# Kernel optimization log

Hardware: AMD Instinct MI355X
Metric: run time of the kernel (lower is better)

Reference implementation:

```python
import jax, jax.numpy as jnp
import numpy as np

DIM = 1024
NUM_HEADS = 16
HEAD_DIM = DIM // NUM_HEADS
B, N = 4, 2048
ROPE_BASE = 10000.0


def _rope_cos_sin(seq_len, dim):
    # inv_freq: (dim/2,), cache layout cat([freqs, freqs], -1) as in the torch module
    inv_freq = 1.0 / (ROPE_BASE ** (jnp.arange(0, dim, 2, dtype=jnp.float32) / dim))
    t = jnp.arange(seq_len, dtype=jnp.float32)
    freqs = jnp.outer(t, inv_freq)                  # (N, dim/2)
    emb = jnp.concatenate([freqs, freqs], axis=-1)  # (N, dim)
    return jnp.cos(emb), jnp.sin(emb)


def _apply_rope(x, cos, sin):
    # x: (B, H, N, Dh); rotation interleaves even/odd lanes: stack([-x_odd, x_even]).flatten
    x_rot = jnp.stack([-x[..., 1::2], x[..., ::2]], axis=-1).reshape(x.shape)
    return x * cos + x_rot * sin


def setup_inputs() -> dict:
    key = jax.random.key(0)
    k1, k2, k3, k4, k5 = jax.random.split(key, 5)
    x = jax.random.normal(k1, (B, N, DIM), dtype=jnp.float32)
    mask = jnp.ones((B, N), dtype=jnp.int32)
    # nn.Linear weights: (out_features, in_features)
    s = 1.0 / np.sqrt(DIM)
    w_qkv = jax.random.uniform(k2, (3 * DIM, DIM), jnp.float32, -s, s)
    b_qkv = jax.random.uniform(k3, (3 * DIM,), jnp.float32, -s, s)
    w_proj = jax.random.uniform(k4, (DIM, DIM), jnp.float32, -s, s)
    b_proj = jax.random.uniform(k5, (DIM,), jnp.float32, -s, s)
    return {"x": x, "mask": mask, "w_qkv": w_qkv, "b_qkv": b_qkv,
            "w_proj": w_proj, "b_proj": b_proj}


def reference(x, mask, w_qkv, b_qkv, w_proj, b_proj):
    Bz, Nz, D = x.shape
    H, Dh = NUM_HEADS, HEAD_DIM
    scale = Dh ** -0.5
    qkv = x @ w_qkv.T + b_qkv                         # (B, N, 3D)
    qkv = qkv.reshape(Bz, Nz, 3, H, Dh)
    qkv = jnp.transpose(qkv, (2, 0, 3, 1, 4))         # (3, B, H, N, Dh)
    q, k, v = qkv[0], qkv[1], qkv[2]
    cos, sin = _rope_cos_sin(Nz, Dh)
    q = _apply_rope(q, cos, sin)
    k = _apply_rope(k, cos, sin)
    attn = jnp.einsum('bhqd,bhkd->bhqk', q, k) * scale
    attn = jnp.where(mask[:, None, None, :] == 0, -jnp.inf, attn)
    attn = jax.nn.softmax(attn, axis=-1)
    out = jnp.einsum('bhqk,bhkd->bhqd', attn, v)      # (B, H, N, Dh)
    out = jnp.transpose(out, (0, 2, 1, 3)).reshape(Bz, Nz, D)
    return out @ w_proj.T + b_proj
```

## Files before the change

### kernel.cpp

```cpp
#include <hip/hip_runtime.h>
#include <hip/hip_bf16.h>

typedef __bf16 bf16;
typedef __attribute__((ext_vector_type(8))) __bf16 bf16x8;
typedef __attribute__((ext_vector_type(4))) __bf16 bf16x4;
typedef __attribute__((ext_vector_type(4))) float f32x4;

#define MFMA16(a, b, c) __builtin_amdgcn_mfma_f32_16x16x32_bf16((a), (b), (c), 0, 0, 0)

__device__ __forceinline__ void gload16(const bf16* g, bf16* lds) {
  __builtin_amdgcn_global_load_lds(
      (const __attribute__((address_space(1))) void*)g,
      (__attribute__((address_space(3))) void*)lds, 16, 0, 0);
}

__global__ void rope_table_kernel(float* __restrict__ cosT, float* __restrict__ sinT) {
  const int n = blockIdx.x;
  const int d = threadIdx.x;
  const int i = d & 31;
  const double inv = pow(10000.0, -(double)(2 * i) / 64.0);
  const float ang = (float)n * (float)inv;
  cosT[n * 64 + d] = cosf(ang);
  sinT[n * 64 + d] = sinf(ang);
}

__global__ void maskbias_kernel(const int* __restrict__ mask, float* __restrict__ mb) {
  const int i = blockIdx.x * blockDim.x + threadIdx.x;
  if (i < 8192) mb[i] = mask[i] ? -4.3280851f : -1e30f;
}

__global__ void cast_f32_bf16(const float* __restrict__ s, bf16* __restrict__ d, int n8) {
  for (int i = blockIdx.x * blockDim.x + threadIdx.x; i < n8; i += gridDim.x * blockDim.x) {
    const float4* p = (const float4*)s + (size_t)i * 2;
    const float4 a = p[0], b = p[1];
    bf16x8 o;
    o[0] = (bf16)a.x; o[1] = (bf16)a.y; o[2] = (bf16)a.z; o[3] = (bf16)a.w;
    o[4] = (bf16)b.x; o[5] = (bf16)b.y; o[6] = (bf16)b.z; o[7] = (bf16)b.w;
    *((bf16x8*)d + i) = o;
  }
}

__device__ __forceinline__ void gemm_tile_1024(const bf16* __restrict__ ga,
                                               const bf16* __restrict__ gb,
                                               bf16* As, bf16* Bs, int t,
                                               f32x4 acc[4][4]) {
  const int l = t & 63;
  const int w = t >> 6, wr = w >> 1, wc = w & 1;
  const int lr = l & 15, lk = (l >> 4) * 8;
  const int r0 = t >> 2, c0 = (t & 3) * 8;
  for (int k0 = 0; k0 < 1024; k0 += 32) {
    gload16(ga + r0 * 1024 + k0 + c0, As + t * 8);
    gload16(ga + (r0 + 64) * 1024 + k0 + c0, As + (t + 256) * 8);
    gload16(gb + r0 * 1024 + k0 + c0, Bs + t * 8);
    gload16(gb + (r0 + 64) * 1024 + k0 + c0, Bs + (t + 256) * 8);
    __syncthreads();
    bf16x8 af[4], bfr[4];
#pragma unroll
    for (int i = 0; i < 4; i++)
      af[i] = *(const bf16x8*)(As + (wr * 64 + i * 16 + lr) * 32 + lk);
#pragma unroll
    for (int j = 0; j < 4; j++)
      bfr[j] = *(const bf16x8*)(Bs + (wc * 64 + j * 16 + lr) * 32 + lk);
#pragma unroll
    for (int i = 0; i < 4; i++)
#pragma unroll
      for (int j = 0; j < 4; j++)
        acc[i][j] = MFMA16(af[i], bfr[j], acc[i][j]);
    __syncthreads();
  }
}

__global__ __launch_bounds__(256) void qkv_rope_kernel(
    const bf16* __restrict__ Xb, const bf16* __restrict__ Wb,
    const float* __restrict__ bias, const float* __restrict__ cosT,
    const float* __restrict__ sinT, bf16* __restrict__ Qo, bf16* __restrict__ Ko,
    bf16* __restrict__ Vo) {
  __shared__ bf16 As[128 * 32];
  __shared__ bf16 Bs[128 * 32];
  __shared__ bf16 Ts[4][16 * 68];
  const int t = threadIdx.x;
  const int m0 = blockIdx.x * 128, o0 = blockIdx.y * 128;
  f32x4 acc[4][4] = {};
  gemm_tile_1024(Xb + (long)m0 * 1024, Wb + (long)o0 * 1024, As, Bs, t, acc);

  const int l = t & 63, w = t >> 6, wr = w >> 1, wc = w & 1;
  const int lr = l & 15, rb = (l >> 4) * 4;
  const int seg = o0 >> 10;
  if (seg < 2) {
    bf16* dst = seg == 0 ? Qo : Ko;
#pragma unroll
    for (int j = 0; j < 4; j++) {
      const int ocol = o0 + wc * 64 + j * 16 + lr;
      const float bv = bias[ocol];
      const int oo = ocol & 1023;
      const int h = oo >> 6, d = oo & 63;
#pragma unroll
      for (int i = 0; i < 4; i++) {
#pragma unroll
        for (int r = 0; r < 4; r++) {
          const int m = m0 + wr * 64 + i * 16 + rb + r;
          const int n = m & 2047, bb = m >> 11;
          float c = acc[i][j][r] + bv;
          const float partner = __shfl_xor(c, 1);
          const float cs = cosT[n * 64 + d], sn = sinT[n * 64 + d];
          c = (d & 1) ? fmaf(c, cs, partner * sn) : fmaf(c, cs, -partner * sn);
          dst[(((long)(bb * 16 + h)) * 2048 + n) * 64 + d] = (bf16)c;
        }
      }
    }
  } else {
    bf16* Tw = &Ts[w][0];
    const int col = l >> 2, chk = l & 3;
    const int mrow = m0 + wr * 64 + chk * 16;
    const int bb2 = mrow >> 11, n2 = mrow & 2047;
#pragma unroll
    for (int j = 0; j < 4; j++) {
      const int ocol = o0 + wc * 64 + j * 16 + lr;
      const float bv = bias[ocol];
#pragma unroll
      for (int i = 0; i < 4; i++)
#pragma unroll
        for (int r = 0; r < 4; r++)
          Tw[lr * 68 + i * 16 + rb + r] = (bf16)(acc[i][j][r] + bv);
      const int oc2 = o0 + wc * 64 + j * 16 + col;
      const int h2 = (oc2 & 1023) >> 6, d2 = oc2 & 63;
      const long vbase = (((long)(bb2 * 16 + h2)) * 64 + d2) * 2048 + n2;
      const bf16x8 v0 = *(const bf16x8*)(Tw + col * 68 + chk * 16);
      const bf16x8 v1 = *(const bf16x8*)(Tw + col * 68 + chk * 16 + 8);
      *(bf16x8*)(Vo + vbase) = v0;
      *(bf16x8*)(Vo + vbase + 8) = v1;
    }
  }
}

__global__ __launch_bounds__(256) void attn_kernel(
    const bf16* __restrict__ Q, const bf16* __restrict__ K, const bf16* __restrict__ Vt,
    const float* __restrict__ mbias, bf16* __restrict__ Aout) {
  __shared__ bf16 Ks[2][64 * 64];
  __shared__ bf16 Vs[2][64 * 64];
  __shared__ bf16 Ps[4][16 * 64];
  const int t = threadIdx.x, l = t & 63, w = t >> 6;
  const int qb = blockIdx.x & 31, h = (blockIdx.x >> 5) & 15, bb = blockIdx.x >> 9;
  const long base = ((long)(bb * 16 + h)) * 2048 * 64;
  const bf16* qp = Q + base;
  const int lr = l & 15, g = l >> 4, rb = g * 4;
  const int q0 = qb * 64 + w * 16;
  bf16* Pw = &Ps[w][0];

  int kaddr[2], pwaddr[4];
#pragma unroll
  for (int ks = 0; ks < 2; ks++) kaddr[ks] = lr * 64 + (((ks * 4 + g) ^ (lr & 7)) * 8);
#pragma unroll
  for (int ct = 0; ct < 4; ct++)
    pwaddr[ct] = lr * 64 + (((ct * 2 + (g >> 1)) ^ (lr & 7)) * 8) + (g & 1) * 4;

  const int rA = (w << 3) + (l >> 3);
  const int sl8 = ((l & 7) ^ (l >> 3)) * 8;
  const int ldsoff = rA * 64 + (l & 7) * 8;
  const bf16* kptr0 = K + base + rA * 64 + sl8;
  const bf16* kptr1 = K + base + (rA + 32) * 64 + sl8;
  const bf16* vptr0 = Vt + base + (long)rA * 2048 + sl8;
  const bf16* vptr1 = Vt + base + (long)(rA + 32) * 2048 + sl8;
  const float* mptr = mbias + bb * 2048 + rb;

  auto stageKV = [&](int buf) {
    gload16(kptr0, &Ks[buf][ldsoff]);
    gload16(kptr1, &Ks[buf][2048 + ldsoff]);
    gload16(vptr0, &Vs[buf][ldsoff]);
    gload16(vptr1, &Vs[buf][2048 + ldsoff]);
    kptr0 += 4096; kptr1 += 4096; vptr0 += 64; vptr1 += 64;
  };

  bf16x8 qf[2];
#pragma unroll
  for (int ks = 0; ks < 2; ks++)
    qf[ks] = *(const bf16x8*)(qp + (q0 + lr) * 64 + ks * 32 + g * 8);

  bf16x8 ones;
#pragma unroll
  for (int i = 0; i < 8; i++) ones[i] = (bf16)1.0f;

  f32x4 oacc[4] = {};
  f32x4 sacc = {};
  const float SCL = 0.18033688f;

  auto compute = [&](const bf16* Kb_, const bf16* Vb_, const float* mp) {
    f32x4 sf[4];
#pragma unroll
    for (int ct = 0; ct < 4; ct++) {
      sf[ct] = (f32x4){0.f, 0.f, 0.f, 0.f};
#pragma unroll
      for (int ks = 0; ks < 2; ks++) {
        const bf16x8 kf = *(const bf16x8*)(Kb_ + ct * 1024 + kaddr[ks]);
        sf[ct] = MFMA16(kf, qf[ks], sf[ct]);
      }
    }
#pragma unroll
    for (int ct = 0; ct < 4; ct++) {
      const float4 mb = *(const float4*)(mp + ct * 16);
      bf16x4 pw;
      pw[0] = (bf16)exp2f(fmaf(sf[ct][0], SCL, mb.x));
      pw[1] = (bf16)exp2f(fmaf(sf[ct][1], SCL, mb.y));
      pw[2] = (bf16)exp2f(fmaf(sf[ct][2], SCL, mb.z));
      pw[3] = (bf16)exp2f(fmaf(sf[ct][3], SCL, mb.w));
      *(bf16x4*)(Pw + pwaddr[ct]) = pw;
    }
#pragma unroll
    for (int ks = 0; ks < 2; ks++) {
      const bf16x8 pf = *(const bf16x8*)(Pw + kaddr[ks]);
      sacc = MFMA16(pf, ones, sacc);
#pragma unroll
      for (int dt = 0; dt < 4; dt++) {
        const bf16x8 vf = *(const bf16x8*)(Vb_ + dt * 1024 + kaddr[ks]);
        oacc[dt] = MFMA16(pf, vf, oacc[dt]);
      }
    }
  };

  stageKV(0);
  for (int it = 0; it < 16; ++it) {
    __syncthreads();
    stageKV(1);
    compute(&Ks[0][0], &Vs[0][0], mptr);
    mptr += 64;
    __syncthreads();
    stageKV(0);
    compute(&Ks[1][0], &Vs[1][0], mptr);
    mptr += 64;
  }

  float li[4];
#pragma unroll
  for (int r = 0; r < 4; r++) li[r] = 1.0f / sacc[r];
#pragma unroll
  for (int dt = 0; dt < 4; dt++)
#pragma unroll
    for (int r = 0; r < 4; r++) {
      const int n = q0 + rb + r;
      Aout[((long)(bb * 2048 + n)) * 1024 + h * 64 + dt * 16 + lr] =
          (bf16)(oacc[dt][r] * li[r]);
    }
}

__global__ __launch_bounds__(256) void proj_kernel(const bf16* __restrict__ Ab,
                                                   const bf16* __restrict__ Wb,
                                                   const float* __restrict__ bias,
                                                   float* __restrict__ out) {
  __shared__ bf16 As[128 * 32];
  __shared__ bf16 Bs[128 * 32];
  const int t = threadIdx.x;
  const int m0 = blockIdx.x * 128, o0 = blockIdx.y * 128;
  f32x4 acc[4][4] = {};
  gemm_tile_1024(Ab + (long)m0 * 1024, Wb + (long)o0 * 1024, As, Bs, t, acc);
  const int l = t & 63, w = t >> 6, wr = w >> 1, wc = w & 1;
  const int lr = l & 15, rb = (l >> 4) * 4;
#pragma unroll
  for (int j = 0; j < 4; j++) {
    const int ocol = o0 + wc * 64 + j * 16 + lr;
    const float bv = bias[ocol];
#pragma unroll
    for (int i = 0; i < 4; i++) {
#pragma unroll
      for (int r = 0; r < 4; r++) {
        const int m = m0 + wr * 64 + i * 16 + rb + r;
        out[(long)m * 1024 + ocol] = acc[i][j][r] + bv;
      }
    }
  }
}

extern "C" void kernel_launch(void* const* d_in, const int* in_sizes, int n_in,
                              void* d_out, int out_size, void* d_ws, size_t ws_size,
                              hipStream_t stream) {
  (void)in_sizes; (void)n_in; (void)out_size; (void)ws_size;
  const float* x = (const float*)d_in[0];
  const int* mask = (const int*)d_in[1];
  const float* w_qkv = (const float*)d_in[2];
  const float* b_qkv = (const float*)d_in[3];
  const float* w_proj = (const float*)d_in[4];
  const float* b_proj = (const float*)d_in[5];
  float* out = (float*)d_out;

  char* ws = (char*)d_ws;
  size_t off = 0;
  auto alloc = [&](size_t bytes) -> void* {
    void* p = ws + off;
    off += (bytes + 255) & ~(size_t)255;
    return p;
  };
  float* cosT = (float*)alloc((size_t)2048 * 64 * 4);
  float* sinT = (float*)alloc((size_t)2048 * 64 * 4);
  float* mbias = (float*)alloc((size_t)8192 * 4);
  bf16* xb = (bf16*)alloc((size_t)8192 * 1024 * 2);
  bf16* wqkvb = (bf16*)alloc((size_t)3072 * 1024 * 2);
  bf16* wprojb = (bf16*)alloc((size_t)1024 * 1024 * 2);
  bf16* Qb = (bf16*)alloc((size_t)8388608 * 2);
  bf16* Kb = (bf16*)alloc((size_t)8388608 * 2);
  bf16* Vb = (bf16*)alloc((size_t)8388608 * 2);
  bf16* A2 = (bf16*)alloc((size_t)8388608 * 2);

  hipLaunchKernelGGL(rope_table_kernel, dim3(2048), dim3(64), 0, stream, cosT, sinT);
  hipLaunchKernelGGL(maskbias_kernel, dim3(32), dim3(256), 0, stream, mask, mbias);
  hipLaunchKernelGGL(cast_f32_bf16, dim3(1024), dim3(256), 0, stream, x, xb, 1048576);
  hipLaunchKernelGGL(cast_f32_bf16, dim3(512), dim3(256), 0, stream, w_qkv, wqkvb, 393216);
  hipLaunchKernelGGL(cast_f32_bf16, dim3(256), dim3(256), 0, stream, w_proj, wprojb, 131072);
  hipLaunchKernelGGL(qkv_rope_kernel, dim3(64, 24), dim3(256), 0, stream, xb, wqkvb,
                     b_qkv, cosT, sinT, Qb, Kb, Vb);
  hipLaunchKernelGGL(attn_kernel, dim3(2048), dim3(256), 0, stream, Qb, Kb, Vb, mbias, A2);
  hipLaunchKernelGGL(proj_kernel, dim3(64, 8), dim3(256), 0, stream, A2, wprojb, b_proj, out);
}
```

Before: 362.1 us.

## Triple-buffer attention K/V with vmcnt waits, stage mask in LDS, remap blocks across XCDs

The attention kernel moves from double to triple buffering of the K/V tiles. It replaces the full __syncthreads with an explicit s_waitcnt vmcnt plus s_barrier, so loads for two tiles ahead stay in flight while the current tile is computed. The mask bias row is copied into LDS once instead of being read from global memory every step. All three GEMM/attention grids are flattened and remapped so blocks are spread across the 8 XCDs for better L2 locality. The cost is more LDS per block (about 48KB for K/V plus 8KB for the mask), which may lower occupancy.

```diff
diff --git a/kernel.cpp b/kernel.cpp
--- a/kernel.cpp
+++ b/kernel.cpp
@@ -79,7 +79,9 @@
   __shared__ bf16 Bs[128 * 32];
   __shared__ bf16 Ts[4][16 * 68];
   const int t = threadIdx.x;
-  const int m0 = blockIdx.x * 128, o0 = blockIdx.y * 128;
+  const int bid = blockIdx.x;
+  const int wid = (bid & 7) * 192 + (bid >> 3);
+  const int m0 = (wid / 24) * 128, o0 = (wid % 24) * 128;
   f32x4 acc[4][4] = {};
   gemm_tile_1024(Xb + (long)m0 * 1024, Wb + (long)o0 * 1024, As, Bs, t, acc);
 
@@ -136,11 +138,13 @@
 __global__ __launch_bounds__(256) void attn_kernel(
     const bf16* __restrict__ Q, const bf16* __restrict__ K, const bf16* __restrict__ Vt,
     const float* __restrict__ mbias, bf16* __restrict__ Aout) {
-  __shared__ bf16 Ks[2][64 * 64];
-  __shared__ bf16 Vs[2][64 * 64];
+  __shared__ bf16 Ks[3][64 * 64];
+  __shared__ bf16 Vs[3][64 * 64];
   __shared__ bf16 Ps[4][16 * 64];
+  __shared__ float Ms[2048];
   const int t = threadIdx.x, l = t & 63, w = t >> 6;
-  const int qb = blockIdx.x & 31, h = (blockIdx.x >> 5) & 15, bb = blockIdx.x >> 9;
+  const int bid = (blockIdx.x & 7) * 256 + (blockIdx.x >> 3);
+  const int qb = bid & 31, h = (bid >> 5) & 15, bb = bid >> 9;
   const long base = ((long)(bb * 16 + h)) * 2048 * 64;
   const bf16* qp = Q + base;
   const int lr = l & 15, g = l >> 4, rb = g * 4;
@@ -161,7 +165,6 @@
   const bf16* kptr1 = K + base + (rA + 32) * 64 + sl8;
   const bf16* vptr0 = Vt + base + (long)rA * 2048 + sl8;
   const bf16* vptr1 = Vt + base + (long)(rA + 32) * 2048 + sl8;
-  const float* mptr = mbias + bb * 2048 + rb;
 
   auto stageKV = [&](int buf) {
     gload16(kptr0, &Ks[buf][ldsoff]);
@@ -176,6 +179,14 @@
   for (int ks = 0; ks < 2; ks++)
     qf[ks] = *(const bf16x8*)(qp + (q0 + lr) * 64 + ks * 32 + g * 8);
 
+  {
+    const float4* src = (const float4*)(mbias + bb * 2048);
+    float4* dstm = (float4*)Ms;
+    dstm[t] = src[t];
+    dstm[t + 256] = src[t + 256];
+  }
+  __syncthreads();
+
   bf16x8 ones;
 #pragma unroll
   for (int i = 0; i < 8; i++) ones[i] = (bf16)1.0f;
@@ -184,7 +195,7 @@
   f32x4 sacc = {};
   const float SCL = 0.18033688f;
 
-  auto compute = [&](const bf16* Kb_, const bf16* Vb_, const float* mp) {
+  auto compute = [&](const bf16* Kb_, const bf16* Vb_, const int kk0) {
     f32x4 sf[4];
 #pragma unroll
     for (int ct = 0; ct < 4; ct++) {
@@ -197,7 +208,7 @@
     }
 #pragma unroll
     for (int ct = 0; ct < 4; ct++) {
-      const float4 mb = *(const float4*)(mp + ct * 16);
+      const float4 mb = *(const float4*)(Ms + kk0 + ct * 16 + rb);
       bf16x4 pw;
       pw[0] = (bf16)exp2f(fmaf(sf[ct][0], SCL, mb.x));
       pw[1] = (bf16)exp2f(fmaf(sf[ct][1], SCL, mb.y));
@@ -218,16 +229,26 @@
   };
 
   stageKV(0);
-  for (int it = 0; it < 16; ++it) {
-    __syncthreads();
-    stageKV(1);
-    compute(&Ks[0][0], &Vs[0][0], mptr);
-    mptr += 64;
-    __syncthreads();
-    stageKV(0);
-    compute(&Ks[1][0], &Vs[1][0], mptr);
-    mptr += 64;
-  }
+  stageKV(1);
+
+  int kk0 = 0;
+#define STEP(CUR, NXT, DOSTAGE, WAITN)                         \
+  {                                                            \
+    asm volatile("s_waitcnt vmcnt(" #WAITN ")" ::: "memory");  \
+    __builtin_amdgcn_s_barrier();                              \
+    asm volatile("" ::: "memory");                             \
+    if (DOSTAGE) stageKV(NXT);                                 \
+    compute(&Ks[CUR][0], &Vs[CUR][0], kk0);                    \
+    kk0 += 64;                                                 \
+  }
+  for (int it = 0; it < 10; ++it) {
+    STEP(0, 2, true, 4);
+    STEP(1, 0, true, 4);
+    STEP(2, 1, true, 4);
+  }
+  STEP(0, 2, false, 4);
+  STEP(1, 0, false, 0);
+#undef STEP
 
   float li[4];
 #pragma unroll
@@ -249,7 +270,9 @@
   __shared__ bf16 As[128 * 32];
   __shared__ bf16 Bs[128 * 32];
   const int t = threadIdx.x;
-  const int m0 = blockIdx.x * 128, o0 = blockIdx.y * 128;
+  const int bid = blockIdx.x;
+  const int wid = (bid & 7) * 64 + (bid >> 3);
+  const int m0 = (wid / 8) * 128, o0 = (wid % 8) * 128;
   f32x4 acc[4][4] = {};
   gemm_tile_1024(Ab + (long)m0 * 1024, Wb + (long)o0 * 1024, As, Bs, t, acc);
   const int l = t & 63, w = t >> 6, wr = w >> 1, wc = w & 1;
@@ -304,8 +327,8 @@
   hipLaunchKernelGGL(cast_f32_bf16, dim3(1024), dim3(256), 0, stream, x, xb, 1048576);
   hipLaunchKernelGGL(cast_f32_bf16, dim3(512), dim3(256), 0, stream, w_qkv, wqkvb, 393216);
   hipLaunchKernelGGL(cast_f32_bf16, dim3(256), dim3(256), 0, stream, w_proj, wprojb, 131072);
-  hipLaunchKernelGGL(qkv_rope_kernel, dim3(64, 24), dim3(256), 0, stream, xb, wqkvb,
+  hipLaunchKernelGGL(qkv_rope_kernel, dim3(1536), dim3(256), 0, stream, xb, wqkvb,
                      b_qkv, cosT, sinT, Qb, Kb, Vb);
   hipLaunchKernelGGL(attn_kernel, dim3(2048), dim3(256), 0, stream, Qb, Kb, Vb, mbias, A2);
-  hipLaunchKernelGGL(proj_kernel, dim3(64, 8), dim3(256), 0, stream, A2, wprojb, b_proj, out);
-}
+  hipLaunchKernelGGL(proj_kernel, dim3(512), dim3(256), 0, stream, A2, wprojb, b_proj, out);
+}
```

New measurement: 355.0 us. 1.02x faster.
